# Optimization experiments

Measured on AMD Instinct MI355X. Metric: run time of the kernel, lower is better.

## Reference

```python
import jax, jax.numpy as jnp
import numpy as np

V, D, H, L, DFF = 32000, 512, 8, 6, 2048
B, T = 64, 256
PAD_IDX = 1


def _pos_encoding(t, d):
    pos = jnp.arange(t, dtype=jnp.float32)[:, None]          # [t,1]
    i2 = jnp.arange(0, d, 2, dtype=jnp.float32)              # [d/2]
    ang = pos / jnp.power(10000.0, i2 / d)                   # [t,d/2]
    pe = jnp.zeros((t, d), dtype=jnp.float32)
    pe = pe.at[:, 0::2].set(jnp.sin(ang))
    pe = pe.at[:, 1::2].set(jnp.cos(ang))
    return pe


def _ln(x, g, b):
    mu = x.mean(-1, keepdims=True)
    var = ((x - mu) ** 2).mean(-1, keepdims=True)
    return (x - mu) * jax.lax.rsqrt(var + 1e-5) * g + b


def _mha(xq, xkv, Wq, Wk, Wv, Wo, bo, causal):
    b, tq, d = xq.shape
    tk = xkv.shape[1]
    hd = d // H
    q = (xq @ Wq).reshape(b, tq, H, hd)
    k = (xkv @ Wk).reshape(b, tk, H, hd)
    v = (xkv @ Wv).reshape(b, tk, H, hd)
    wei = jnp.einsum('bqhd,bkhd->bhqk', q, k) * (hd ** -0.5)
    if causal:
        mask = jnp.tril(jnp.ones((tq, tk), dtype=bool))
        wei = jnp.where(mask, wei, -jnp.inf)
    wei = jax.nn.softmax(wei, axis=-1)
    out = jnp.einsum('bhqk,bkhd->bqhd', wei, v).reshape(b, tq, d)
    return out @ Wo + bo


def _ffn(x, W1, b1, W2, b2):
    return jax.nn.relu(x @ W1 + b1) @ W2 + b2


def setup_inputs() -> dict:
    key = jax.random.key(0)
    ks = iter(jax.random.split(key, 64))
    nrm = lambda shape: (jax.random.normal(next(ks), shape, dtype=jnp.float32) * 0.02)
    inp = {
        'idx': jax.random.randint(next(ks), (B, T), 0, V),
        'idx_enc': jax.random.randint(next(ks), (B, T), 0, V),
        'targets': jax.random.randint(next(ks), (B, T), 0, V),
        'emb_dec': nrm((V, D)),
        'emb_enc': nrm((V, D)),
        # encoder stacks [L, ...]
        'enc_Wq': nrm((L, D, D)), 'enc_Wk': nrm((L, D, D)), 'enc_Wv': nrm((L, D, D)),
        'enc_Wo': nrm((L, D, D)), 'enc_bo': jnp.zeros((L, D)),
        'enc_ln_g': jnp.ones((L, 2, D)), 'enc_ln_b': jnp.zeros((L, 2, D)),
        'enc_W1': nrm((L, D, DFF)), 'enc_b1': jnp.zeros((L, DFF)),
        'enc_W2': nrm((L, DFF, D)), 'enc_b2': jnp.zeros((L, D)),
        # decoder stacks [L, ...]
        'dec_Wq_sa': nrm((L, D, D)), 'dec_Wk_sa': nrm((L, D, D)), 'dec_Wv_sa': nrm((L, D, D)),
        'dec_Wo_sa': nrm((L, D, D)), 'dec_bo_sa': jnp.zeros((L, D)),
        'dec_Wq_xa': nrm((L, D, D)), 'dec_Wk_xa': nrm((L, D, D)), 'dec_Wv_xa': nrm((L, D, D)),
        'dec_Wo_xa': nrm((L, D, D)), 'dec_bo_xa': jnp.zeros((L, D)),
        'dec_ln_g': jnp.ones((L, 4, D)), 'dec_ln_b': jnp.zeros((L, 4, D)),
        'dec_W1': nrm((L, D, DFF)), 'dec_b1': jnp.zeros((L, DFF)),
        'dec_W2': nrm((L, DFF, D)), 'dec_b2': jnp.zeros((L, D)),
        'lnf_g': jnp.ones((D,)), 'lnf_b': jnp.zeros((D,)),
        'Wlm': nrm((D, V)), 'blm': jnp.zeros((V,)),
    }
    return inp


def reference(idx, idx_enc, targets, emb_dec, emb_enc,
              enc_Wq, enc_Wk, enc_Wv, enc_Wo, enc_bo, enc_ln_g, enc_ln_b,
              enc_W1, enc_b1, enc_W2, enc_b2,
              dec_Wq_sa, dec_Wk_sa, dec_Wv_sa, dec_Wo_sa, dec_bo_sa,
              dec_Wq_xa, dec_Wk_xa, dec_Wv_xa, dec_Wo_xa, dec_bo_xa,
              dec_ln_g, dec_ln_b, dec_W1, dec_b1, dec_W2, dec_b2,
              lnf_g, lnf_b, Wlm, blm):
    t_dec = idx.shape[1]
    t_enc = idx_enc.shape[1]
    pe = _pos_encoding(256, D)
    # encoder
    y = emb_enc[idx_enc] + pe[:t_enc]
    for l in range(L):
        h = _ln(y, enc_ln_g[l, 0], enc_ln_b[l, 0])
        y = y + _mha(h, h, enc_Wq[l], enc_Wk[l], enc_Wv[l], enc_Wo[l], enc_bo[l], causal=False)
        h = _ln(y, enc_ln_g[l, 1], enc_ln_b[l, 1])
        y = y + _ffn(h, enc_W1[l], enc_b1[l], enc_W2[l], enc_b2[l])
    # decoder
    x = emb_dec[idx] + pe[:t_dec]
    for l in range(L):
        h = _ln(x, dec_ln_g[l, 0], dec_ln_b[l, 0])
        x = x + _mha(h, h, dec_Wq_sa[l], dec_Wk_sa[l], dec_Wv_sa[l], dec_Wo_sa[l], dec_bo_sa[l], causal=True)
        hq = _ln(x, dec_ln_g[l, 1], dec_ln_b[l, 1])
        hk = _ln(y, dec_ln_g[l, 2], dec_ln_b[l, 2])
        x = x + _mha(hq, hk, dec_Wq_xa[l], dec_Wk_xa[l], dec_Wv_xa[l], dec_Wo_xa[l], dec_bo_xa[l], causal=False)
        h = _ln(x, dec_ln_g[l, 3], dec_ln_b[l, 3])
        x = x + _ffn(h, dec_W1[l], dec_b1[l], dec_W2[l], dec_b2[l])
    x = _ln(x, lnf_g, lnf_b)
    logits = (x @ Wlm + blm).reshape(-1, V)  # [B*T, V]
    # cross entropy with ignore_index = PAD_IDX, mean over non-ignored
    tgt = targets.reshape(-1)
    logp = jax.nn.log_softmax(logits, axis=-1)
    nll = -jnp.take_along_axis(logp, tgt[:, None], axis=-1)[:, 0]
    valid = (tgt != PAD_IDX).astype(logits.dtype)
    loss = jnp.sum(nll * valid) / jnp.maximum(jnp.sum(valid), 1.0)
    return logits, loss
```

## Files before the change

### kernel.cpp

```cpp
#include <hip/hip_runtime.h>

typedef __attribute__((ext_vector_type(8))) short s8v;
typedef __attribute__((ext_vector_type(4))) float f4v;
using u16 = unsigned short;
using u8 = unsigned char;

__device__ __forceinline__ u16 f2bf(float f) {
  union { float f; unsigned u; } v; v.f = f;
  return (u16)((v.u + 0x7FFFu + ((v.u >> 16) & 1u)) >> 16);
}

__device__ __forceinline__ u8 f2f8(float f) {
  union { float f; unsigned u; } v; v.f = f;
  unsigned s = (v.u >> 24) & 0x80;
  v.u &= 0x7fffffff;
  if (!(v.f < 448.f)) return (u8)(s | 0x7e);
  if (v.f < 0.015625f) {
    int q = (int)(v.f * 512.f + 0.5f);
    return (u8)(s | (unsigned)q);
  }
  unsigned u = v.u + 0x7FFFFu + ((v.u >> 20) & 1u);
  int e = (int)(u >> 23) - 127;
  unsigned m = (u >> 20) & 7u;
  unsigned code = ((unsigned)(e + 7) << 3) | m;
  if (code > 0x7e) code = 0x7e;
  return (u8)(s | code);
}

__global__ __launch_bounds__(256) void pe_kernel(float* __restrict__ pe) {
  int i = blockIdx.x * 256 + threadIdx.x;
  int t = i >> 8, p = i & 255;
  float ex = (2.f * (float)p) / 512.f;
  float ang = (float)t * expf(-ex * 9.210340371976184f);
  pe[t * 512 + 2 * p]     = sinf(ang);
  pe[t * 512 + 2 * p + 1] = cosf(ang);
}

template<int FP8>
__global__ __launch_bounds__(256) void wconv_kernel(const float* __restrict__ in,
    void* __restrict__ out, int R, int C, size_t dstride) {
  __shared__ float tile[64][65];
  const size_t mat = (size_t)R * C;
  const float* src = in + (size_t)blockIdx.z * mat;
  int r0 = blockIdx.x * 64, c0 = blockIdx.y * 64;
  int tr = threadIdx.x >> 6, tc = threadIdx.x & 63;
#pragma unroll
  for (int i = 0; i < 16; ++i)
    tile[i * 4 + tr][tc] = src[(size_t)(r0 + i * 4 + tr) * C + (c0 + tc)];
  __syncthreads();
#pragma unroll
  for (int i = 0; i < 16; ++i) {
    size_t di = (size_t)(c0 + i * 4 + tr) * R + (r0 + tc);
    float val = tile[tc][i * 4 + tr];
    if (FP8) ((u8*)out + (size_t)blockIdx.z * dstride)[di] = f2f8(val);
    else     ((u16*)out + (size_t)blockIdx.z * dstride)[di] = f2bf(val);
  }
}

struct WcSq { const float* src[12]; void* dst[12]; unsigned long long dstr[12]; unsigned fp8m; };
__global__ __launch_bounds__(256) void wconv_sq_kernel(WcSq S) {
  __shared__ float tile[64][65];
  int mm = blockIdx.z / 6, l = blockIdx.z % 6;
  const float* src = S.src[mm] + (size_t)l * 512 * 512;
  int fp8 = (S.fp8m >> mm) & 1;
  int r0 = blockIdx.x * 64, c0 = blockIdx.y * 64;
  int tr = threadIdx.x >> 6, tc = threadIdx.x & 63;
#pragma unroll
  for (int i = 0; i < 16; ++i)
    tile[i * 4 + tr][tc] = src[(size_t)(r0 + i * 4 + tr) * 512 + (c0 + tc)];
  __syncthreads();
#pragma unroll
  for (int i = 0; i < 16; ++i) {
    size_t di = (size_t)(c0 + i * 4 + tr) * 512 + (r0 + tc);
    float val = tile[tc][i * 4 + tr];
    if (fp8) ((u8*)S.dst[mm] + (size_t)l * S.dstr[mm])[di] = f2f8(val);
    else     ((u16*)S.dst[mm] + (size_t)l * S.dstr[mm])[di] = f2bf(val);
  }
}

template<int FP8>
__device__ __forceinline__ void ln_row(f4v v0, f4v v1, const float* g, const float* b,
                                       int lane, void* outrow) {
  float s = v0[0] + v0[1] + v0[2] + v0[3] + v1[0] + v1[1] + v1[2] + v1[3];
#pragma unroll
  for (int o = 1; o < 64; o <<= 1) s += __shfl_xor(s, o);
  float mu = s * (1.f / 512.f);
  float q = 0.f;
#pragma unroll
  for (int j = 0; j < 4; ++j) {
    float d0 = v0[j] - mu; q += d0 * d0;
    float d1 = v1[j] - mu; q += d1 * d1;
  }
#pragma unroll
  for (int o = 1; o < 64; o <<= 1) q += __shfl_xor(q, o);
  float rs = rsqrtf(q * (1.f / 512.f) + 1e-5f);
  f4v g0 = *(const f4v*)(g + lane * 8), g1 = *(const f4v*)(g + lane * 8 + 4);
  f4v b0 = *(const f4v*)(b + lane * 8), b1 = *(const f4v*)(b + lane * 8 + 4);
  if (FP8) {
    unsigned long long ov = 0;
#pragma unroll
    for (int j = 0; j < 4; ++j) {
      ov |= (unsigned long long)f2f8((v0[j] - mu) * rs * g0[j] + b0[j]) << (8 * j);
      ov |= (unsigned long long)f2f8((v1[j] - mu) * rs * g1[j] + b1[j]) << (8 * (4 + j));
    }
    *(unsigned long long*)((u8*)outrow + lane * 8) = ov;
  } else {
    s8v ov;
#pragma unroll
    for (int j = 0; j < 4; ++j) {
      ov[j]     = (short)f2bf((v0[j] - mu) * rs * g0[j] + b0[j]);
      ov[4 + j] = (short)f2bf((v1[j] - mu) * rs * g1[j] + b1[j]);
    }
    *(s8v*)((u16*)outrow + lane * 8) = ov;
  }
}

template<int FP8>
__global__ __launch_bounds__(256) void ln_kernel(const float* __restrict__ x,
    const float* __restrict__ g, const float* __restrict__ b, void* __restrict__ out) {
  int row = blockIdx.x * 4 + (threadIdx.x >> 6);
  int lane = threadIdx.x & 63;
  const float* xr = x + (size_t)row * 512 + lane * 8;
  void* orow = FP8 ? (void*)((u8*)out + (size_t)row * 512)
                   : (void*)((u16*)out + (size_t)row * 512);
  ln_row<FP8>(*(const f4v*)xr, *(const f4v*)(xr + 4), g, b, lane, orow);
}

__global__ __launch_bounds__(256) void ln2_kernel(
    const float* __restrict__ x1, const float* __restrict__ g1, const float* __restrict__ b1,
    u16* __restrict__ o1, const float* __restrict__ x2, const float* __restrict__ g2,
    const float* __restrict__ b2, u16* __restrict__ o2) {
  int row = blockIdx.x * 4 + (threadIdx.x >> 6);
  int lane = threadIdx.x & 63;
  const float* x = x1; const float* g = g1; const float* b = b1; u16* o = o1;
  if (row >= 16384) { row -= 16384; x = x2; g = g2; b = b2; o = o2; }
  const float* xr = x + (size_t)row * 512 + lane * 8;
  ln_row<0>(*(const f4v*)xr, *(const f4v*)(xr + 4), g, b, lane, o + (size_t)row * 512);
}

__global__ __launch_bounds__(256) void emb_ln_kernel(const int* __restrict__ idx,
    const float* __restrict__ emb, const float* __restrict__ pe,
    const float* __restrict__ g, const float* __restrict__ b,
    float* __restrict__ y, u16* __restrict__ h) {
  int row = blockIdx.x * 4 + (threadIdx.x >> 6);
  int lane = threadIdx.x & 63;
  int tok = idx[row], t = row & 255;
  const float* e = emb + (size_t)tok * 512 + lane * 8;
  const float* p = pe + (size_t)t * 512 + lane * 8;
  f4v v0 = *(const f4v*)e + *(const f4v*)p;
  f4v v1 = *(const f4v*)(e + 4) + *(const f4v*)(p + 4);
  float* yr = y + (size_t)row * 512 + lane * 8;
  *(f4v*)yr = v0; *(f4v*)(yr + 4) = v1;
  ln_row<0>(v0, v1, g, b, lane, h + (size_t)row * 512);
}

template<int AB8, int OMODE, int HAS_BIAS, int ADD_RES, int RELU, int WLOSS,
         int NT, int SWZM, int DUAL>
__global__ __launch_bounds__(256, 4) void gemm128(
    const void* __restrict__ Av, const void* __restrict__ Btv,
    const float* __restrict__ bias, const float* __restrict__ res,
    void* __restrict__ outp, int M, int N, int K,
    float* __restrict__ pmax, float* __restrict__ psum,
    const void* __restrict__ A2, const void* __restrict__ Bt2,
    void* __restrict__ out2) {
  __shared__ __align__(16) u8 smem[32768];
  const int tid = threadIdx.x, lane = tid & 63, w = tid >> 6;
  int bx, by;
  if (SWZM == 1) {
    int flat = blockIdx.y * gridDim.x + blockIdx.x;
    int xcd = flat & 7, local = flat >> 3;
    int p = local / gridDim.y;
    by = local - p * gridDim.y;
    bx = xcd * (gridDim.x >> 3) + p;
  } else {
    int nx = gridDim.x;
    int flat = blockIdx.y * nx + blockIdx.x;
    int per = (nx * gridDim.y) >> 3;
    int sw = (flat & 7) * per + (flat >> 3);
    by = sw / nx; bx = sw - by * nx;
  }
  const void* Ause = Av; const void* Buse = Btv; void* Ouse = outp;
  int Nn = N;
  if (DUAL && by >= 4) { Ause = A2; Buse = Bt2; Ouse = out2; Nn = 1024; by -= 4; }
  const int m0 = bx * 128, n0 = by * 128;
  const int wm = (w >> 1) * 64, wn = (w & 1) * 64;
  const int lhi = lane >> 4, llo = lane & 15;
  const int srow = tid >> 3, sl = tid & 7;

  f4v acc[4][4] = {};

  if (AB8) {
    const u8* A = (const u8*)Ause;
    const u8* Bt = (const u8*)Buse;
    u8* As8 = smem;
    u8* Bs8 = smem + 16384;
    const int gcolb = (sl ^ (srow & 7)) * 16;
    const u8* Ag = A + (size_t)(m0 + srow) * K + gcolb;
    const u8* Bg = Bt + (size_t)(n0 + srow) * K + gcolb;
    const size_t rstep = (size_t)32 * K;
    const int sxb = llo & 7;
    const int nk = K >> 7;
    for (int t = 0; t < nk; ++t) {
      const int kt = t * 128;
#pragma unroll
      for (int q = 0; q < 4; ++q)
        __builtin_amdgcn_global_load_lds(
            (const __attribute__((address_space(1))) void*)(Ag + q * rstep + kt),
            (__attribute__((address_space(3))) void*)(&As8[(q * 32 + srow) * 128 + sl * 16]),
            16, 0, 0);
#pragma unroll
      for (int q = 0; q < 4; ++q)
        __builtin_amdgcn_global_load_lds(
            (const __attribute__((address_space(1))) void*)(Bg + q * rstep + kt),
            (__attribute__((address_space(3))) void*)(&Bs8[(q * 32 + srow) * 128 + sl * 16]),
            16, 0, 0);
      __syncthreads();
#pragma unroll
      for (int kk = 0; kk < 4; ++kk) {
        const int slot8 = kk * 4 + lhi;
        const int lbyte = (((slot8 >> 1) ^ sxb) * 16) + ((slot8 & 1) * 8);
        long af[4], bf8[4];
#pragma unroll
        for (int i = 0; i < 4; ++i)
          af[i] = *(const long*)&As8[(wm + i * 16 + llo) * 128 + lbyte];
#pragma unroll
        for (int j = 0; j < 4; ++j)
          bf8[j] = *(const long*)&Bs8[(wn + j * 16 + llo) * 128 + lbyte];
#pragma unroll
        for (int i = 0; i < 4; ++i)
#pragma unroll
          for (int j = 0; j < 4; ++j)
            acc[i][j] = __builtin_amdgcn_mfma_f32_16x16x32_fp8_fp8(af[i], bf8[j], acc[i][j], 0, 0, 0);
      }
      __syncthreads();
    }
  } else {
    const u16* A = (const u16*)Ause;
    const u16* Bt = (const u16*)Buse;
    u16* As = (u16*)smem;
    u16* Bs = (u16*)(smem + 16384);
    const int gcol = (sl ^ (srow & 7)) * 8;
    const u16* Ag = A + (size_t)(m0 + srow) * K + gcol;
    const u16* Bg = Bt + (size_t)(n0 + srow) * K + gcol;
    const size_t rstep = (size_t)32 * K;
    const int sx = llo & 7;
    const int nk = K >> 6;
    for (int t = 0; t < nk; ++t) {
      const int kt = t * 64;
#pragma unroll
      for (int q = 0; q < 4; ++q)
        __builtin_amdgcn_global_load_lds(
            (const __attribute__((address_space(1))) void*)(Ag + q * rstep + kt),
            (__attribute__((address_space(3))) void*)(&As[(q * 32 + srow) * 64 + sl * 8]),
            16, 0, 0);
#pragma unroll
      for (int q = 0; q < 4; ++q)
        __builtin_amdgcn_global_load_lds(
            (const __attribute__((address_space(1))) void*)(Bg + q * rstep + kt),
            (__attribute__((address_space(3))) void*)(&Bs[(q * 32 + srow) * 64 + sl * 8]),
            16, 0, 0);
      __syncthreads();
#pragma unroll
      for (int kk = 0; kk < 2; ++kk) {
        s8v af[4], bfv[4];
#pragma unroll
        for (int i = 0; i < 4; ++i)
          af[i] = *(const s8v*)&As[(wm + i * 16 + llo) * 64 + (((kk * 4 + lhi) ^ sx) * 8)];
#pragma unroll
        for (int j = 0; j < 4; ++j)
          bfv[j] = *(const s8v*)&Bs[(wn + j * 16 + llo) * 64 + (((kk * 4 + lhi) ^ sx) * 8)];
#pragma unroll
        for (int i = 0; i < 4; ++i)
#pragma unroll
          for (int j = 0; j < 4; ++j)
            acc[i][j] = __builtin_amdgcn_mfma_f32_16x16x32_bf16(af[i], bfv[j], acc[i][j], 0, 0, 0);
      }
      __syncthreads();
    }
  }

  if (OMODE == 1 || OMODE == 2) {
    float bvj[4];
#pragma unroll
    for (int j = 0; j < 4; ++j)
      bvj[j] = HAS_BIAS ? bias[n0 + wn + j * 16 + llo] : 0.f;
#pragma unroll
    for (int i = 0; i < 4; ++i) {
#pragma unroll
      for (int j = 0; j < 4; ++j) {
        int col = n0 + wn + j * 16 + llo;
#pragma unroll
        for (int r = 0; r < 4; ++r) {
          int row = m0 + wm + i * 16 + lhi * 4 + r;
          float v = acc[i][j][r] + bvj[j];
          if (RELU) v = fmaxf(v, 0.f);
          if (OMODE == 1) ((u16*)Ouse)[(size_t)row * Nn + col] = f2bf(v);
          else            ((u8*)Ouse)[(size_t)row * Nn + col] = f2f8(v);
        }
      }
    }
  } else {
    float* lb = (float*)smem;
    float* wbuf = lb + w * 1088;
    float* lbm = lb + 4608;
    float* lbs = lb + 4864;
    f4v bias4 = {0.f, 0.f, 0.f, 0.f};
    if (HAS_BIAS) bias4 = *(const f4v*)(bias + n0 + wn + llo * 4);
#pragma unroll
    for (int i = 0; i < 4; ++i) {
#pragma unroll
      for (int j = 0; j < 4; ++j)
#pragma unroll
        for (int r = 0; r < 4; ++r)
          wbuf[(lhi * 4 + r) * 68 + j * 16 + llo] = acc[i][j][r];
      asm volatile("s_waitcnt lgkmcnt(0)" ::: "memory");
      __builtin_amdgcn_sched_barrier(0);
#pragma unroll
      for (int p = 0; p < 4; ++p) {
        int r16 = p * 4 + lhi;
        f4v v4 = *(const f4v*)&wbuf[r16 * 68 + llo * 4];
        v4 += bias4;
        int grow = m0 + wm + i * 16 + r16;
        int gcol4 = n0 + wn + llo * 4;
        if (ADD_RES) v4 += *(const f4v*)(res + (size_t)grow * Nn + gcol4);
        if (RELU) {
          v4[0] = fmaxf(v4[0], 0.f); v4[1] = fmaxf(v4[1], 0.f);
          v4[2] = fmaxf(v4[2], 0.f); v4[3] = fmaxf(v4[3], 0.f);
        }
        float* dst = (float*)Ouse + (size_t)grow * Nn + gcol4;
        if (NT) __builtin_nontemporal_store(v4, (f4v*)dst);
        else    *(f4v*)dst = v4;
        if (WLOSS) {
          float mx = fmaxf(fmaxf(v4[0], v4[1]), fmaxf(v4[2], v4[3]));
          mx = fmaxf(mx, __shfl_xor(mx, 1));
          mx = fmaxf(mx, __shfl_xor(mx, 2));
          mx = fmaxf(mx, __shfl_xor(mx, 4));
          mx = fmaxf(mx, __shfl_xor(mx, 8));
          float sum = __expf(v4[0] - mx) + __expf(v4[1] - mx)
                    + __expf(v4[2] - mx) + __expf(v4[3] - mx);
          sum += __shfl_xor(sum, 1); sum += __shfl_xor(sum, 2);
          sum += __shfl_xor(sum, 4); sum += __shfl_xor(sum, 8);
          if (llo == 0) {
            int lr = wm + i * 16 + r16;
            lbm[lr * 2 + (wn >> 6)] = mx;
            lbs[lr * 2 + (wn >> 6)] = sum;
          }
        }
      }
      asm volatile("s_waitcnt lgkmcnt(0)" ::: "memory");
      __builtin_amdgcn_sched_barrier(0);
    }
    if (WLOSS) {
      __syncthreads();
      if (tid < 128) {
        float ma = lbm[tid * 2], mb = lbm[tid * 2 + 1];
        float sa = lbs[tid * 2], sb = lbs[tid * 2 + 1];
        float m = fmaxf(ma, mb);
        float ss = sa * __expf(ma - m) + sb * __expf(mb - m);
        int ntile = Nn >> 7;
        pmax[(size_t)(m0 + tid) * ntile + by] = m;
        psum[(size_t)(m0 + tid) * ntile + by] = ss;
      }
    }
  }
}

__global__ __launch_bounds__(256, 2) void attn_kernel(
    const u16* __restrict__ Qp, int qs, const u16* __restrict__ Kp,
    const u16* __restrict__ Vp, int kvs, u8* __restrict__ Ob, int causal) {
  __shared__ __align__(16) u16 Ks[64][72];
  __shared__ __align__(16) u16 Vt[64][66];
  __shared__ __align__(16) u16 Ps[4][16][66];
  const int tid = threadIdx.x, lane = tid & 63, w = tid >> 6;
  const int b = blockIdx.x >> 3, h = blockIdx.x & 7;
  const size_t qbase  = (size_t)b * 256 * qs  + (size_t)h * 64;
  const size_t kvbase = (size_t)b * 256 * kvs + (size_t)h * 64;
  const size_t obase  = (size_t)b * 256 * 512 + (size_t)h * 64;
  const int lhi = lane >> 4, llo = lane & 15;
  s8v aq0[4], aq1[4];
#pragma unroll
  for (int qc = 0; qc < 4; ++qc) {
    const u16* qp = Qp + qbase + (size_t)(w * 64 + qc * 16 + llo) * qs;
    aq0[qc] = *(const s8v*)(qp + lhi * 8);
    aq1[qc] = *(const s8v*)(qp + 32 + lhi * 8);
  }
  f4v o[4][4] = {};
  float mrow[16], lrow[16];
#pragma unroll
  for (int i = 0; i < 16; ++i) { mrow[i] = -1e30f; lrow[i] = 0.f; }

  for (int kt = 0; kt < 4; ++kt) {
    if (kt) __syncthreads();
    {
      int tr = tid >> 3, d0 = (tid & 7) * 8;
#pragma unroll
      for (int it = 0; it < 2; ++it) {
        int t = it * 32 + tr;
        const u16* kp = Kp + kvbase + (size_t)(kt * 64 + t) * kvs + d0;
        *(s8v*)&Ks[t][d0] = *(const s8v*)kp;
        s8v vv = *(const s8v*)(Vp + kvbase + (size_t)(kt * 64 + t) * kvs + d0);
#pragma unroll
        for (int j = 0; j < 8; ++j) Vt[d0 + j][t] = (u16)vv[j];
      }
    }
    __syncthreads();
#pragma unroll
    for (int qc = 0; qc < 4; ++qc) {
      if (causal && kt * 64 > w * 64 + qc * 16 + 15) continue;
      f4v S[4];
#pragma unroll
      for (int c = 0; c < 4; ++c) {
        s8v bk0 = *(const s8v*)&Ks[c * 16 + llo][lhi * 8];
        s8v bk1 = *(const s8v*)&Ks[c * 16 + llo][32 + lhi * 8];
        f4v z = {0.f, 0.f, 0.f, 0.f};
        z = __builtin_amdgcn_mfma_f32_16x16x32_bf16(aq0[qc], bk0, z, 0, 0, 0);
        S[c] = __builtin_amdgcn_mfma_f32_16x16x32_bf16(aq1[qc], bk1, z, 0, 0, 0);
      }
      float scv[4];
#pragma unroll
      for (int r = 0; r < 4; ++r) {
        const int tq = w * 64 + qc * 16 + lhi * 4 + r;
        float tmax = -1e30f;
#pragma unroll
        for (int c = 0; c < 4; ++c) {
          float s = S[c][r] * 0.125f;
          if (causal && (kt * 64 + c * 16 + llo) > tq) s = -1e30f;
          S[c][r] = s;
          tmax = fmaxf(tmax, s);
        }
        tmax = fmaxf(tmax, __shfl_xor(tmax, 1));
        tmax = fmaxf(tmax, __shfl_xor(tmax, 2));
        tmax = fmaxf(tmax, __shfl_xor(tmax, 4));
        tmax = fmaxf(tmax, __shfl_xor(tmax, 8));
        float mo = mrow[qc * 4 + r];
        float mn = fmaxf(mo, tmax);
        float sc = __expf(mo - mn);
        float sum = 0.f;
#pragma unroll
        for (int c = 0; c < 4; ++c) {
          float p = __expf(S[c][r] - mn);
          sum += p;
          Ps[w][lhi * 4 + r][c * 16 + llo] = f2bf(p);
        }
        sum += __shfl_xor(sum, 1); sum += __shfl_xor(sum, 2);
        sum += __shfl_xor(sum, 4); sum += __shfl_xor(sum, 8);
        lrow[qc * 4 + r] = lrow[qc * 4 + r] * sc + sum;
        mrow[qc * 4 + r] = mn;
        scv[r] = sc;
      }
#pragma unroll
      for (int nb = 0; nb < 4; ++nb)
#pragma unroll
        for (int r = 0; r < 4; ++r)
          o[qc][nb][r] *= scv[r];
      asm volatile("s_waitcnt lgkmcnt(0)" ::: "memory");
      __builtin_amdgcn_sched_barrier(0);
#pragma unroll
      for (int kb = 0; kb < 2; ++kb) {
        s8v pa = *(const s8v*)&Ps[w][llo][kb * 32 + lhi * 8];
#pragma unroll
        for (int nb = 0; nb < 4; ++nb) {
          s8v bv = *(const s8v*)&Vt[nb * 16 + llo][kb * 32 + lhi * 8];
          o[qc][nb] = __builtin_amdgcn_mfma_f32_16x16x32_bf16(pa, bv, o[qc][nb], 0, 0, 0);
        }
      }
    }
  }
#pragma unroll
  for (int qc = 0; qc < 4; ++qc)
#pragma unroll
    for (int nb = 0; nb < 4; ++nb)
#pragma unroll
      for (int r = 0; r < 4; ++r) {
        float inv = 1.f / lrow[qc * 4 + r];
        Ob[obase + (size_t)(w * 64 + qc * 16 + lhi * 4 + r) * 512 + nb * 16 + llo] =
            f2f8(o[qc][nb][r] * inv);
      }
}

__global__ __launch_bounds__(256) void loss_lse_kernel(const float* __restrict__ pmax,
    const float* __restrict__ psum, const float* __restrict__ logits,
    const int* __restrict__ tgt, float* __restrict__ nll, float* __restrict__ valid) {
  const int w = threadIdx.x >> 6, lane = threadIdx.x & 63;
  const int row = blockIdx.x * 4 + w;
  float m = -1e30f, s = 0.f;
  for (int e = lane; e < 250; e += 64) {
    float pm = pmax[(size_t)row * 250 + e], ps = psum[(size_t)row * 250 + e];
    if (pm > m) { s = s * __expf(m - pm) + ps; m = pm; }
    else          s += ps * __expf(pm - m);
  }
#pragma unroll
  for (int o = 1; o < 64; o <<= 1) {
    float om = __shfl_xor(m, o), os = __shfl_xor(s, o);
    float mm = fmaxf(m, om);
    s = s * __expf(m - mm) + os * __expf(om - mm);
    m = mm;
  }
  if (lane == 0) {
    int t = tgt[row];
    float lse = m + logf(s);
    float v = (t != 1) ? 1.f : 0.f;
    nll[row] = v * (lse - logits[(size_t)row * 32000 + t]);
    valid[row] = v;
  }
}

__global__ __launch_bounds__(256) void loss_final_kernel(const float* __restrict__ nll,
    const float* __restrict__ valid, float* __restrict__ out) {
  __shared__ float sa[256], sb[256];
  int tid = threadIdx.x;
  float s = 0.f, c = 0.f;
  for (int i = tid; i < 16384; i += 256) { s += nll[i]; c += valid[i]; }
  sa[tid] = s; sb[tid] = c;
  __syncthreads();
  for (int st = 128; st > 0; st >>= 1) {
    if (tid < st) { sa[tid] += sa[tid + st]; sb[tid] += sb[tid + st]; }
    __syncthreads();
  }
  if (tid == 0) out[0] = sa[0] / fmaxf(sb[0], 1.f);
}

extern "C" void kernel_launch(void* const* d_in, const int* in_sizes, int n_in,
                              void* d_out, int out_size, void* d_ws, size_t ws_size,
                              hipStream_t stream) {
  (void)in_sizes; (void)n_in; (void)out_size; (void)ws_size;
  const int* idx       = (const int*)d_in[0];
  const int* idx_enc   = (const int*)d_in[1];
  const int* targets   = (const int*)d_in[2];
  const float* emb_dec = (const float*)d_in[3];
  const float* emb_enc = (const float*)d_in[4];
  const float* enc_Wq  = (const float*)d_in[5];
  const float* enc_Wk  = (const float*)d_in[6];
  const float* enc_Wv  = (const float*)d_in[7];
  const float* enc_Wo  = (const float*)d_in[8];
  const float* enc_bo  = (const float*)d_in[9];
  const float* enc_ln_g = (const float*)d_in[10];
  const float* enc_ln_b = (const float*)d_in[11];
  const float* enc_W1  = (const float*)d_in[12];
  const float* enc_b1  = (const float*)d_in[13];
  const float* enc_W2  = (const float*)d_in[14];
  const float* enc_b2  = (const float*)d_in[15];
  const float* dWq_sa  = (const float*)d_in[16];
  const float* dWk_sa  = (const float*)d_in[17];
  const float* dWv_sa  = (const float*)d_in[18];
  const float* dWo_sa  = (const float*)d_in[19];
  const float* dbo_sa  = (const float*)d_in[20];
  const float* dWq_xa  = (const float*)d_in[21];
  const float* dWk_xa  = (const float*)d_in[22];
  const float* dWv_xa  = (const float*)d_in[23];
  const float* dWo_xa  = (const float*)d_in[24];
  const float* dbo_xa  = (const float*)d_in[25];
  const float* dec_ln_g = (const float*)d_in[26];
  const float* dec_ln_b = (const float*)d_in[27];
  const float* dec_W1  = (const float*)d_in[28];
  const float* dec_b1  = (const float*)d_in[29];
  const float* dec_W2  = (const float*)d_in[30];
  const float* dec_b2  = (const float*)d_in[31];
  const float* lnf_g   = (const float*)d_in[32];
  const float* lnf_b   = (const float*)d_in[33];
  const float* Wlm     = (const float*)d_in[34];
  const float* blm     = (const float*)d_in[35];
  float* out_logits = (float*)d_out;
  float* out_loss   = out_logits + (size_t)16384 * 32000;

  size_t off = 0;
  auto alloc = [&](size_t bytes) -> char* {
    char* p = (char*)d_ws + off;
    off += (bytes + 255) & ~(size_t)255;
    return p;
  };
  const size_t SQ = 512 * 512, SF = 512 * 2048;
  u16* tWqkvE = (u16*)alloc(6 * 3 * SQ * 2);
  u8*  tWoE   = (u8*)alloc(6 * SQ);
  u8*  tW1E   = (u8*)alloc(6 * SF);
  u8*  tW2E   = (u8*)alloc(6 * SF);
  u16* tWqkvS = (u16*)alloc(6 * 3 * SQ * 2);
  u8*  tWoS   = (u8*)alloc(6 * SQ);
  u16* tWqX   = (u16*)alloc(6 * SQ * 2);
  u16* tWkvX  = (u16*)alloc(6 * 2 * SQ * 2);
  u8*  tWoX   = (u8*)alloc(6 * SQ);
  u8*  tW1D   = (u8*)alloc(6 * SF);
  u8*  tW2D   = (u8*)alloc(6 * SF);
  u16* tWlm   = (u16*)alloc((size_t)32000 * 512 * 2);
  float* pe   = (float*)alloc(256 * 512 * 4);
  float* yE   = (float*)alloc((size_t)16384 * 512 * 4);
  float* xD   = (float*)alloc((size_t)16384 * 512 * 4);
  u16* hA     = (u16*)alloc((size_t)16384 * 512 * 2);
  u16* hB     = (u16*)alloc((size_t)16384 * 512 * 2);
  u16* qkvB   = (u16*)alloc((size_t)16384 * 1536 * 2);
  u16* qB     = (u16*)alloc((size_t)16384 * 512 * 2);
  u16* kvB    = (u16*)alloc((size_t)16384 * 1024 * 2);
  u8*  atB    = (u8*)alloc((size_t)16384 * 512);
  u8*  midB   = (u8*)alloc((size_t)16384 * 2048);
  float* pmax = (float*)alloc((size_t)16384 * 250 * 4);
  float* psum = (float*)alloc((size_t)16384 * 250 * 4);
  float* rnll = (float*)alloc(16384 * 4);
  float* rval = (float*)alloc(16384 * 4);

  dim3 tb(256);
  const size_t S3 = 3 * SQ, S2 = 2 * SQ;
  {
    WcSq S;
    S.src[0] = enc_Wq;  S.dst[0] = tWqkvE + 0 * SQ; S.dstr[0] = S3;
    S.src[1] = enc_Wk;  S.dst[1] = tWqkvE + 1 * SQ; S.dstr[1] = S3;
    S.src[2] = enc_Wv;  S.dst[2] = tWqkvE + 2 * SQ; S.dstr[2] = S3;
    S.src[3] = enc_Wo;  S.dst[3] = tWoE;            S.dstr[3] = SQ;
    S.src[4] = dWq_sa;  S.dst[4] = tWqkvS + 0 * SQ; S.dstr[4] = S3;
    S.src[5] = dWk_sa;  S.dst[5] = tWqkvS + 1 * SQ; S.dstr[5] = S3;
    S.src[6] = dWv_sa;  S.dst[6] = tWqkvS + 2 * SQ; S.dstr[6] = S3;
    S.src[7] = dWo_sa;  S.dst[7] = tWoS;            S.dstr[7] = SQ;
    S.src[8] = dWq_xa;  S.dst[8] = tWqX;            S.dstr[8] = SQ;
    S.src[9] = dWk_xa;  S.dst[9] = tWkvX + 0 * SQ;  S.dstr[9] = S2;
    S.src[10] = dWv_xa; S.dst[10] = tWkvX + 1 * SQ; S.dstr[10] = S2;
    S.src[11] = dWo_xa; S.dst[11] = tWoX;           S.dstr[11] = SQ;
    S.fp8m = (1u << 3) | (1u << 7) | (1u << 11);
    wconv_sq_kernel<<<dim3(8, 8, 72), tb, 0, stream>>>(S);
  }
  wconv_kernel<1><<<dim3(8, 32, 6), tb, 0, stream>>>(enc_W1, tW1E, 512, 2048, SF);
  wconv_kernel<1><<<dim3(32, 8, 6), tb, 0, stream>>>(enc_W2, tW2E, 2048, 512, SF);
  wconv_kernel<1><<<dim3(8, 32, 6), tb, 0, stream>>>(dec_W1, tW1D, 512, 2048, SF);
  wconv_kernel<1><<<dim3(32, 8, 6), tb, 0, stream>>>(dec_W2, tW2D, 2048, 512, SF);
  wconv_kernel<0><<<dim3(8, 500, 1), tb, 0, stream>>>(Wlm, tWlm, 512, 32000, (size_t)0);
  pe_kernel<<<256, 256, 0, stream>>>(pe);

  auto ln16 = [&](const float* xin, const float* g, const float* bb, u16* o) {
    ln_kernel<0><<<4096, 256, 0, stream>>>(xin, g, bb, o);
  };
  auto ln8 = [&](const float* xin, const float* g, const float* bb, void* o) {
    ln_kernel<1><<<4096, 256, 0, stream>>>(xin, g, bb, o);
  };
  auto g_bf16 = [&](const u16* Ap, const u16* Bp, u16* Op, int N) {
    gemm128<0, 1, 0, 0, 0, 0, 0, 0, 0><<<dim3(128, N / 128), 256, 0, stream>>>(
        Ap, Bp, nullptr, nullptr, Op, 16384, N, 512, nullptr, nullptr,
        nullptr, nullptr, nullptr);
  };
  auto g_qkv_x = [&](const u16* Aq, const u16* Bq, u16* Oq,
                     const u16* Akv, const u16* Bkv, u16* Okv) {
    gemm128<0, 1, 0, 0, 0, 0, 0, 0, 1><<<dim3(128, 12), 256, 0, stream>>>(
        Aq, Bq, nullptr, nullptr, Oq, 16384, 512, 512, nullptr, nullptr,
        Akv, Bkv, Okv);
  };
  auto proj_res8 = [&](const u8* Ap, const u8* Bp, const float* bi, float* xr, int K) {
    gemm128<1, 0, 1, 1, 0, 0, 0, 0, 0><<<dim3(128, 4), 256, 0, stream>>>(
        Ap, Bp, bi, xr, xr, 16384, 512, K, nullptr, nullptr,
        nullptr, nullptr, nullptr);
  };
  auto ffn1_8 = [&](const u8* Ap, const u8* Bp, const float* bi, u8* Op) {
    gemm128<1, 2, 1, 0, 1, 0, 0, 0, 0><<<dim3(128, 16), 256, 0, stream>>>(
        Ap, Bp, bi, nullptr, Op, 16384, 2048, 512, nullptr, nullptr,
        nullptr, nullptr, nullptr);
  };

  emb_ln_kernel<<<4096, 256, 0, stream>>>(idx_enc, emb_enc, pe,
      enc_ln_g + 0, enc_ln_b + 0, yE, hA);
  for (int l = 0; l < 6; ++l) {
    if (l) ln16(yE, enc_ln_g + (l * 2 + 0) * 512, enc_ln_b + (l * 2 + 0) * 512, hA);
    g_bf16(hA, tWqkvE + l * S3, qkvB, 1536);
    attn_kernel<<<512, 256, 0, stream>>>(qkvB, 1536, qkvB + 512, qkvB + 1024, 1536, atB, 0);
    proj_res8(atB, tWoE + l * SQ, enc_bo + l * 512, yE, 512);
    ln8(yE, enc_ln_g + (l * 2 + 1) * 512, enc_ln_b + (l * 2 + 1) * 512, hA);
    ffn1_8((const u8*)hA, tW1E + l * SF, enc_b1 + l * 2048, midB);
    proj_res8(midB, tW2E + l * SF, enc_b2 + l * 512, yE, 2048);
  }

  emb_ln_kernel<<<4096, 256, 0, stream>>>(idx, emb_dec, pe,
      dec_ln_g + 0, dec_ln_b + 0, xD, hA);
  for (int l = 0; l < 6; ++l) {
    if (l) ln16(xD, dec_ln_g + (l * 4 + 0) * 512, dec_ln_b + (l * 4 + 0) * 512, hA);
    g_bf16(hA, tWqkvS + l * S3, qkvB, 1536);
    attn_kernel<<<512, 256, 0, stream>>>(qkvB, 1536, qkvB + 512, qkvB + 1024, 1536, atB, 1);
    proj_res8(atB, tWoS + l * SQ, dbo_sa + l * 512, xD, 512);
    ln2_kernel<<<8192, 256, 0, stream>>>(
        xD, dec_ln_g + (l * 4 + 1) * 512, dec_ln_b + (l * 4 + 1) * 512, hA,
        yE, dec_ln_g + (l * 4 + 2) * 512, dec_ln_b + (l * 4 + 2) * 512, hB);
    g_qkv_x(hA, tWqX + l * SQ, qB, hB, tWkvX + l * S2, kvB);
    attn_kernel<<<512, 256, 0, stream>>>(qB, 512, kvB, kvB + 512, 1024, atB, 0);
    proj_res8(atB, tWoX + l * SQ, dbo_xa + l * 512, xD, 512);
    ln8(xD, dec_ln_g + (l * 4 + 3) * 512, dec_ln_b + (l * 4 + 3) * 512, hA);
    ffn1_8((const u8*)hA, tW1D + l * SF, dec_b1 + l * 2048, midB);
    proj_res8(midB, tW2D + l * SF, dec_b2 + l * 512, xD, 2048);
  }

  ln16(xD, lnf_g, lnf_b, hA);
  gemm128<0, 0, 1, 0, 0, 1, 1, 1, 0><<<dim3(128, 250), 256, 0, stream>>>(
      hA, tWlm, blm, nullptr, out_logits, 16384, 32000, 512, pmax, psum,
      nullptr, nullptr, nullptr);
  loss_lse_kernel<<<4096, 256, 0, stream>>>(pmax, psum, out_logits, targets, rnll, rval);
  loss_final_kernel<<<1, 256, 0, stream>>>(rnll, rval, out_loss);
}
```

Baseline: 4.498 ms.

## Store residual streams in bf16 instead of fp32

The encoder and decoder residual buffers (yE, xD) change from fp32 to bf16. Embedding, layernorm and residual-add projection kernels now read and write bf16, and a new output mode in the GEMM epilogue adds a bf16 residual and writes bf16. This halves the memory traffic of the residual stream in every layer. The cost is extra rounding error that builds up across the residual adds over 12 layers, which could put the outputs outside tolerance.

```diff
diff --git a/kernel.cpp b/kernel.cpp
--- a/kernel.cpp
+++ b/kernel.cpp
@@ -2,12 +2,17 @@
 
 typedef __attribute__((ext_vector_type(8))) short s8v;
 typedef __attribute__((ext_vector_type(4))) float f4v;
+typedef __attribute__((ext_vector_type(4))) unsigned short us4;
 using u16 = unsigned short;
 using u8 = unsigned char;
 
 __device__ __forceinline__ u16 f2bf(float f) {
   union { float f; unsigned u; } v; v.f = f;
   return (u16)((v.u + 0x7FFFu + ((v.u >> 16) & 1u)) >> 16);
+}
+__device__ __forceinline__ float b2f(u16 x) {
+  union { unsigned u; float f; } v; v.u = (unsigned)x << 16;
+  return v.f;
 }
 
 __device__ __forceinline__ u8 f2f8(float f) {
@@ -115,33 +120,44 @@
   }
 }
 
+__device__ __forceinline__ void ldbf16x8(const u16* p, f4v& v0, f4v& v1) {
+  s8v raw = *(const s8v*)p;
+#pragma unroll
+  for (int j = 0; j < 4; ++j) {
+    v0[j] = b2f((u16)raw[j]);
+    v1[j] = b2f((u16)raw[4 + j]);
+  }
+}
+
 template<int FP8>
-__global__ __launch_bounds__(256) void ln_kernel(const float* __restrict__ x,
+__global__ __launch_bounds__(256) void ln_kernel(const u16* __restrict__ x,
     const float* __restrict__ g, const float* __restrict__ b, void* __restrict__ out) {
   int row = blockIdx.x * 4 + (threadIdx.x >> 6);
   int lane = threadIdx.x & 63;
-  const float* xr = x + (size_t)row * 512 + lane * 8;
+  f4v v0, v1;
+  ldbf16x8(x + (size_t)row * 512 + lane * 8, v0, v1);
   void* orow = FP8 ? (void*)((u8*)out + (size_t)row * 512)
                    : (void*)((u16*)out + (size_t)row * 512);
-  ln_row<FP8>(*(const f4v*)xr, *(const f4v*)(xr + 4), g, b, lane, orow);
+  ln_row<FP8>(v0, v1, g, b, lane, orow);
 }
 
 __global__ __launch_bounds__(256) void ln2_kernel(
-    const float* __restrict__ x1, const float* __restrict__ g1, const float* __restrict__ b1,
-    u16* __restrict__ o1, const float* __restrict__ x2, const float* __restrict__ g2,
+    const u16* __restrict__ x1, const float* __restrict__ g1, const float* __restrict__ b1,
+    u16* __restrict__ o1, const u16* __restrict__ x2, const float* __restrict__ g2,
     const float* __restrict__ b2, u16* __restrict__ o2) {
   int row = blockIdx.x * 4 + (threadIdx.x >> 6);
   int lane = threadIdx.x & 63;
-  const float* x = x1; const float* g = g1; const float* b = b1; u16* o = o1;
+  const u16* x = x1; const float* g = g1; const float* b = b1; u16* o = o1;
   if (row >= 16384) { row -= 16384; x = x2; g = g2; b = b2; o = o2; }
-  const float* xr = x + (size_t)row * 512 + lane * 8;
-  ln_row<0>(*(const f4v*)xr, *(const f4v*)(xr + 4), g, b, lane, o + (size_t)row * 512);
+  f4v v0, v1;
+  ldbf16x8(x + (size_t)row * 512 + lane * 8, v0, v1);
+  ln_row<0>(v0, v1, g, b, lane, o + (size_t)row * 512);
 }
 
 __global__ __launch_bounds__(256) void emb_ln_kernel(const int* __restrict__ idx,
     const float* __restrict__ emb, const float* __restrict__ pe,
     const float* __restrict__ g, const float* __restrict__ b,
-    float* __restrict__ y, u16* __restrict__ h) {
+    u16* __restrict__ y, u16* __restrict__ h) {
   int row = blockIdx.x * 4 + (threadIdx.x >> 6);
   int lane = threadIdx.x & 63;
   int tok = idx[row], t = row & 255;
@@ -149,8 +165,13 @@
   const float* p = pe + (size_t)t * 512 + lane * 8;
   f4v v0 = *(const f4v*)e + *(const f4v*)p;
   f4v v1 = *(const f4v*)(e + 4) + *(const f4v*)(p + 4);
-  float* yr = y + (size_t)row * 512 + lane * 8;
-  *(f4v*)yr = v0; *(f4v*)(yr + 4) = v1;
+  s8v yv;
+#pragma unroll
+  for (int j = 0; j < 4; ++j) {
+    yv[j] = (short)f2bf(v0[j]);
+    yv[4 + j] = (short)f2bf(v1[j]);
+  }
+  *(s8v*)(y + (size_t)row * 512 + lane * 8) = yv;
   ln_row<0>(v0, v1, g, b, lane, h + (size_t)row * 512);
 }
 
@@ -158,7 +179,7 @@
          int NT, int SWZM, int DUAL>
 __global__ __launch_bounds__(256, 4) void gemm128(
     const void* __restrict__ Av, const void* __restrict__ Btv,
-    const float* __restrict__ bias, const float* __restrict__ res,
+    const float* __restrict__ bias, const void* __restrict__ res,
     void* __restrict__ outp, int M, int N, int K,
     float* __restrict__ pmax, float* __restrict__ psum,
     const void* __restrict__ A2, const void* __restrict__ Bt2,
@@ -322,28 +343,43 @@
         v4 += bias4;
         int grow = m0 + wm + i * 16 + r16;
         int gcol4 = n0 + wn + llo * 4;
-        if (ADD_RES) v4 += *(const f4v*)(res + (size_t)grow * Nn + gcol4);
-        if (RELU) {
-          v4[0] = fmaxf(v4[0], 0.f); v4[1] = fmaxf(v4[1], 0.f);
-          v4[2] = fmaxf(v4[2], 0.f); v4[3] = fmaxf(v4[3], 0.f);
-        }
-        float* dst = (float*)Ouse + (size_t)grow * Nn + gcol4;
-        if (NT) __builtin_nontemporal_store(v4, (f4v*)dst);
-        else    *(f4v*)dst = v4;
-        if (WLOSS) {
-          float mx = fmaxf(fmaxf(v4[0], v4[1]), fmaxf(v4[2], v4[3]));
-          mx = fmaxf(mx, __shfl_xor(mx, 1));
-          mx = fmaxf(mx, __shfl_xor(mx, 2));
-          mx = fmaxf(mx, __shfl_xor(mx, 4));
-          mx = fmaxf(mx, __shfl_xor(mx, 8));
-          float sum = __expf(v4[0] - mx) + __expf(v4[1] - mx)
-                    + __expf(v4[2] - mx) + __expf(v4[3] - mx);
-          sum += __shfl_xor(sum, 1); sum += __shfl_xor(sum, 2);
-          sum += __shfl_xor(sum, 4); sum += __shfl_xor(sum, 8);
-          if (llo == 0) {
-            int lr = wm + i * 16 + r16;
-            lbm[lr * 2 + (wn >> 6)] = mx;
-            lbs[lr * 2 + (wn >> 6)] = sum;
+        if (OMODE == 3) {
+          if (ADD_RES) {
+            us4 rv = *(const us4*)((const u16*)res + (size_t)grow * Nn + gcol4);
+#pragma unroll
+            for (int j = 0; j < 4; ++j) v4[j] += b2f(rv[j]);
+          }
+          if (RELU) {
+            v4[0] = fmaxf(v4[0], 0.f); v4[1] = fmaxf(v4[1], 0.f);
+            v4[2] = fmaxf(v4[2], 0.f); v4[3] = fmaxf(v4[3], 0.f);
+          }
+          us4 ov;
+#pragma unroll
+          for (int j = 0; j < 4; ++j) ov[j] = f2bf(v4[j]);
+          *(us4*)((u16*)Ouse + (size_t)grow * Nn + gcol4) = ov;
+        } else {
+          if (RELU) {
+            v4[0] = fmaxf(v4[0], 0.f); v4[1] = fmaxf(v4[1], 0.f);
+            v4[2] = fmaxf(v4[2], 0.f); v4[3] = fmaxf(v4[3], 0.f);
+          }
+          float* dst = (float*)Ouse + (size_t)grow * Nn + gcol4;
+          if (NT) __builtin_nontemporal_store(v4, (f4v*)dst);
+          else    *(f4v*)dst = v4;
+          if (WLOSS) {
+            float mx = fmaxf(fmaxf(v4[0], v4[1]), fmaxf(v4[2], v4[3]));
+            mx = fmaxf(mx, __shfl_xor(mx, 1));
+            mx = fmaxf(mx, __shfl_xor(mx, 2));
+            mx = fmaxf(mx, __shfl_xor(mx, 4));
+            mx = fmaxf(mx, __shfl_xor(mx, 8));
+            float sum = __expf(v4[0] - mx) + __expf(v4[1] - mx)
+                      + __expf(v4[2] - mx) + __expf(v4[3] - mx);
+            sum += __shfl_xor(sum, 1); sum += __shfl_xor(sum, 2);
+            sum += __shfl_xor(sum, 4); sum += __shfl_xor(sum, 8);
+            if (llo == 0) {
+              int lr = wm + i * 16 + r16;
+              lbm[lr * 2 + (wn >> 6)] = mx;
+              lbs[lr * 2 + (wn >> 6)] = sum;
+            }
           }
         }
       }
@@ -583,8 +619,8 @@
   u8*  tW2D   = (u8*)alloc(6 * SF);
   u16* tWlm   = (u16*)alloc((size_t)32000 * 512 * 2);
   float* pe   = (float*)alloc(256 * 512 * 4);
-  float* yE   = (float*)alloc((size_t)16384 * 512 * 4);
-  float* xD   = (float*)alloc((size_t)16384 * 512 * 4);
+  u16* yE     = (u16*)alloc((size_t)16384 * 512 * 2);
+  u16* xD     = (u16*)alloc((size_t)16384 * 512 * 2);
   u16* hA     = (u16*)alloc((size_t)16384 * 512 * 2);
   u16* hB     = (u16*)alloc((size_t)16384 * 512 * 2);
   u16* qkvB   = (u16*)alloc((size_t)16384 * 1536 * 2);
@@ -623,10 +659,10 @@
   wconv_kernel<0><<<dim3(8, 500, 1), tb, 0, stream>>>(Wlm, tWlm, 512, 32000, (size_t)0);
   pe_kernel<<<256, 256, 0, stream>>>(pe);
 
-  auto ln16 = [&](const float* xin, const float* g, const float* bb, u16* o) {
+  auto ln16 = [&](const u16* xin, const float* g, const float* bb, u16* o) {
     ln_kernel<0><<<4096, 256, 0, stream>>>(xin, g, bb, o);
   };
-  auto ln8 = [&](const float* xin, const float* g, const float* bb, void* o) {
+  auto ln8 = [&](const u16* xin, const float* g, const float* bb, void* o) {
     ln_kernel<1><<<4096, 256, 0, stream>>>(xin, g, bb, o);
   };
   auto g_bf16 = [&](const u16* Ap, const u16* Bp, u16* Op, int N) {
@@ -640,8 +676,8 @@
         Aq, Bq, nullptr, nullptr, Oq, 16384, 512, 512, nullptr, nullptr,
         Akv, Bkv, Okv);
   };
-  auto proj_res8 = [&](const u8* Ap, const u8* Bp, const float* bi, float* xr, int K) {
-    gemm128<1, 0, 1, 1, 0, 0, 0, 0, 0><<<dim3(128, 4), 256, 0, stream>>>(
+  auto proj_res8 = [&](const u8* Ap, const u8* Bp, const float* bi, u16* xr, int K) {
+    gemm128<1, 3, 1, 1, 0, 0, 0, 0, 0><<<dim3(128, 4), 256, 0, stream>>>(
         Ap, Bp, bi, xr, xr, 16384, 512, K, nullptr, nullptr,
         nullptr, nullptr, nullptr);
   };
```

After: 4.322 ms. 3.9% less time.
